# Performance work log

Measured on AMD Instinct MI355X. Metric: run time of the kernel, lower is better.

The kernel has to match this reference:

```python
import jax, jax.numpy as jnp
import numpy as np

C = 343.0      # speed of sound (init kwarg c)
F = 16         # number of frequency channels (len(omega))
H = 128        # MLP hidden width
N = 131072     # collocation points


def _mlp(coords, W1, b1, W2, b2, W3, b3):
    # coords: [..., 3] -> [..., 2F] (first F = real part, last F = imag part)
    h = jnp.tanh(coords @ W1 + b1)
    h = jnp.tanh(h @ W2 + b2)
    return h @ W3 + b3


def setup_inputs() -> dict:
    key = jax.random.key(0)
    ks = jax.random.split(key, 4)
    inputs = jax.random.normal(ks[0], (N, 3), dtype=jnp.float32)
    # omega = 2*pi*f for f = 100..1600 Hz (matches init kwarg list)
    omega = 2.0 * jnp.pi * 100.0 * jnp.arange(1, F + 1, dtype=jnp.float32)
    s_in = 1.0 / np.sqrt(3.0)
    s_h = 1.0 / np.sqrt(float(H))
    W1 = jax.random.normal(ks[1], (3, H), dtype=jnp.float32) * s_in
    b1 = jnp.zeros((H,), dtype=jnp.float32)
    W2 = jax.random.normal(ks[2], (H, H), dtype=jnp.float32) * s_h
    b2 = jnp.zeros((H,), dtype=jnp.float32)
    W3 = jax.random.normal(ks[3], (H, 2 * F), dtype=jnp.float32) * s_h
    b3 = jnp.zeros((2 * F,), dtype=jnp.float32)
    return {"inputs": inputs, "omega": omega, "W1": W1, "b1": b1,
            "W2": W2, "b2": b2, "W3": W3, "b3": b3}


def reference(inputs, omega, W1, b1, W2, b2, W3, b3):
    # Pointwise network R^3 -> R^{2F} (real/imag stacked).
    f = lambda c3: _mlp(c3, W1, b1, W2, b2, W3, b3)

    # u: complex pressure per point per frequency, [N, F]
    out = _mlp(inputs, W1, b1, W2, b2, W3, b3)           # [N, 2F]
    u = out[:, :F] + 1j * out[:, F:]

    # Full spatial Hessian per point via forward-over-reverse AD (fused
    # replacement for the torch per-channel autograd.grad loop).
    hess = jax.vmap(jax.jacfwd(jax.jacrev(f)))(inputs)   # [N, 2F, 3, 3]
    lap_ri = jnp.einsum('nfii->nf', hess)                # diagonal trace = Laplacian
    lap = lap_ri[:, :F] + 1j * lap_ri[:, F:]             # [N, F] complex

    # PDE residual skips channel 0, exactly as the torch loop (i+1 indexing).
    k2 = (omega[1:] / C) ** 2                            # [F-1]
    residual = lap[:, 1:] + k2 * u[:, 1:]                # [N, F-1]

    # mean over channels then over batch == global mean of |residual|^2
    return jnp.mean(jnp.abs(residual) ** 2)
```

## Files before the change

### kernel.cpp

```cpp
#include <hip/hip_runtime.h>
#include <math.h>

#ifndef __has_builtin
#define __has_builtin(x) 0
#endif

#define NPTS   131072
#define FCH    16
#define CSND   343.0f
#define PB     16
#define BLOCK  256
#define GRID   512
#define NBLK   (NPTS / PB)

typedef _Float16 half8 __attribute__((ext_vector_type(8)));
typedef _Float16 half2v __attribute__((ext_vector_type(2)));
typedef float    f32x4 __attribute__((ext_vector_type(4)));

static __device__ __forceinline__ unsigned pack2(float a, float b) {
#if __has_builtin(__builtin_amdgcn_cvt_pkrtz)
  return __builtin_bit_cast(unsigned, __builtin_amdgcn_cvt_pkrtz(a, b));
#else
  half2v v; v[0] = (_Float16)a; v[1] = (_Float16)b;
  return __builtin_bit_cast(unsigned, v);
#endif
}

static __device__ __forceinline__ float mytanh(float x) {
  float ax = fabsf(x);
  float e  = __expf(-2.0f * ax);
  float r  = (1.0f - e) * __builtin_amdgcn_rcpf(1.0f + e);
  return copysignf(r, x);
}


__global__ __launch_bounds__(BLOCK, 2) void helmholtz_kernel(
    const float* __restrict__ x,
    const float* __restrict__ omega,
    const float* __restrict__ W1,
    const float* __restrict__ b1,
    const float* __restrict__ W2,
    const float* __restrict__ b2,
    const float* __restrict__ W3,
    const float* __restrict__ b3,
    float* __restrict__ out)
{
  __shared__ unsigned s_w2t[128 * 64];
  __shared__ unsigned s_w3t[32 * 64];
  __shared__ unsigned s_A[80 * 64];

  const int tid  = threadIdx.x;
  const int w    = tid >> 6;
  const int l    = tid & 63;
  const int col  = l & 15;
  const int quad = l >> 4;

  for (int task = tid; task < 2048; task += BLOCK) {
    int n = task & 127, c = task >> 7;
    unsigned pk[4];
#pragma unroll
    for (int d = 0; d < 4; d++)
      pk[d] = pack2(W2[(8 * c + 2 * d) * 128 + n], W2[(8 * c + 2 * d + 1) * 128 + n]);
    uint4 q = make_uint4(pk[0], pk[1], pk[2], pk[3]);
    *(uint4*)&s_w2t[n * 64 + ((c ^ (n & 15)) << 2)] = q;
  }
  for (int task = tid; task < 512; task += BLOCK) {
    int n = task & 31, c = task >> 5;
    unsigned pk[4];
#pragma unroll
    for (int d = 0; d < 4; d++)
      pk[d] = pack2(W3[(8 * c + 2 * d) * 32 + n], W3[(8 * c + 2 * d + 1) * 32 + n]);
    uint4 q = make_uint4(pk[0], pk[1], pk[2], pk[3]);
    *(uint4*)&s_w3t[n * 64 + ((c ^ (n & 15)) << 2)] = q;
  }

  const int i2 = tid & 63;
  const float a0x = W1[2 * i2],       a0y = W1[128 + 2 * i2],  a0z = W1[256 + 2 * i2];
  const float a1x = W1[2 * i2 + 1],   a1y = W1[129 + 2 * i2],  a1z = W1[257 + 2 * i2];
  const float bb0 = b1[2 * i2],       bb1 = b1[2 * i2 + 1];
  const float wsq0 = a0x * a0x + a0y * a0y + a0z * a0z;
  const float wsq1 = a1x * a1x + a1y * a1y + a1z * a1z;
  const float b2r0 = b2[w * 32 + col];
  const float b2r1 = b2[w * 32 + 16 + col];
  const bool  activeE = (tid & 15) < 15;
  const int   cE = (tid & 15) + 1;
  float k2E = 0.0f, b3a = 0.0f, b3b = 0.0f;
  if (activeE) {
    float om = omega[cE] * (1.0f / CSND);
    k2E = om * om;
    b3a = b3[cE];
    b3b = b3[cE + 16];
  }

  float wsum = 0.0f;

  for (int blk = blockIdx.x; blk < NBLK; blk += gridDim.x) {
    const int pbase = blk * PB;
    __syncthreads();

#pragma unroll
    for (int it = 0; it < 4; it++) {
      int p = (tid >> 6) * 4 + it;
      const float* xp = x + (size_t)(pbase + p) * 3;
      float x0 = xp[0], x1 = xp[1], x2 = xp[2];
      float z0 = fmaf(x0, a0x, fmaf(x1, a0y, fmaf(x2, a0z, bb0)));
      float z1 = fmaf(x0, a1x, fmaf(x1, a1y, fmaf(x2, a1z, bb1)));
      float t0 = mytanh(z0), t1 = mytanh(z1);
      float s0 = 1.0f - t0 * t0, s1 = 1.0f - t1 * t1;
      unsigned u_h  = pack2(t0, t1);
      unsigned u_d0 = pack2(s0 * a0x, s1 * a1x);
      unsigned u_d1 = pack2(s0 * a0y, s1 * a1y);
      unsigned u_d2 = pack2(s0 * a0z, s1 * a1z);
      unsigned u_c  = pack2(-2.0f * t0 * s0 * wsq0, -2.0f * t1 * s1 * wsq1);
      int dcol = (((i2 >> 2) ^ p) << 2) + (i2 & 3);
      s_A[(p)      * 64 + dcol] = u_h;
      s_A[(16 + p) * 64 + dcol] = u_d0;
      s_A[(32 + p) * 64 + dcol] = u_d1;
      s_A[(48 + p) * 64 + dcol] = u_d2;
      s_A[(64 + p) * 64 + dcol] = u_c;
    }
    __syncthreads();

    f32x4 acc[5][2];
#pragma unroll
    for (int mt = 0; mt < 5; mt++)
#pragma unroll
      for (int ntl = 0; ntl < 2; ntl++)
        acc[mt][ntl] = (f32x4){0.0f, 0.0f, 0.0f, 0.0f};

    half8 bfrag[2][4];
#pragma unroll
    for (int ntl = 0; ntl < 2; ntl++) {
      int n = (2 * w + ntl) * 16 + col;
#pragma unroll
      for (int ks = 0; ks < 4; ks++) {
        int c = (ks * 4 + quad) ^ (n & 15);
        bfrag[ntl][ks] = *(const half8*)&s_w2t[n * 64 + (c << 2)];
      }
    }
#pragma unroll
    for (int mt = 0; mt < 5; mt++) {
      int m = mt * 16 + col;
#pragma unroll
      for (int ks = 0; ks < 4; ks++) {
        int c = (ks * 4 + quad) ^ (m & 15);
        half8 af = *(const half8*)&s_A[m * 64 + (c << 2)];
        acc[mt][0] = __builtin_amdgcn_mfma_f32_16x16x32_f16(af, bfrag[0][ks], acc[mt][0], 0, 0, 0);
        acc[mt][1] = __builtin_amdgcn_mfma_f32_16x16x32_f16(af, bfrag[1][ks], acc[mt][1], 0, 0, 0);
      }
    }
    __syncthreads();

    {
      _Float16* hg = (_Float16*)s_A;
#pragma unroll
      for (int ntl = 0; ntl < 2; ntl++) {
        int j = (2 * w + ntl) * 16 + col;
        int chunkj = j >> 3;
        float b2v = ntl ? b2r1 : b2r0;
#pragma unroll
        for (int r = 0; r < 4; r++) {
          int p = quad * 4 + r;
          float z2 = acc[0][ntl][r] + b2v;
          float d0 = acc[1][ntl][r], d1 = acc[2][ntl][r], d2 = acc[3][ntl][r];
          float Av = acc[4][ntl][r];
          float t2 = mytanh(z2);
          float s2 = 1.0f - t2 * t2;
          float g  = s2 * (Av - 2.0f * t2 * (d0 * d0 + d1 * d1 + d2 * d2));
          int base = ((chunkj ^ p) << 3) + (j & 7);
          hg[p * 128 + base]        = (_Float16)t2;
          hg[(16 + p) * 128 + base] = (_Float16)g;
        }
      }
    }
    __syncthreads();

    {
      int mtp = w >> 1, ntp = w & 1;
      int mrow = mtp * 16 + col;
      int n    = ntp * 16 + col;
      f32x4 dacc = (f32x4){0.0f, 0.0f, 0.0f, 0.0f};
#pragma unroll
      for (int ks = 0; ks < 4; ks++) {
        int ca = (ks * 4 + quad) ^ (mrow & 15);
        half8 af = *(const half8*)&s_A[mrow * 64 + (ca << 2)];
        int cb = (ks * 4 + quad) ^ (n & 15);
        half8 bf = *(const half8*)&s_w3t[n * 64 + (cb << 2)];
        dacc = __builtin_amdgcn_mfma_f32_16x16x32_f16(af, bf, dacc, 0, 0, 0);
      }
      float* ylds = (float*)&s_A[2048];
      int base = mtp ? 528 : 0;
#pragma unroll
      for (int r = 0; r < 4; r++) {
        int p = quad * 4 + r;
        ylds[base + p * 33 + ntp * 16 + col] = dacc[r];
      }
    }
    __syncthreads();

    if (activeE) {
      const float* ylds = (const float*)&s_A[2048];
      int p = tid >> 4;
      float yre = ylds[p * 33 + cE] + b3a;
      float yim = ylds[p * 33 + cE + 16] + b3b;
      float lre = ylds[528 + p * 33 + cE];
      float lim = ylds[528 + p * 33 + cE + 16];
      float re = fmaf(k2E, yre, lre);
      float im = fmaf(k2E, yim, lim);
      wsum += re * re + im * im;
    }
  }

#pragma unroll
  for (int off = 32; off > 0; off >>= 1)
    wsum += __shfl_down(wsum, off, 64);
  if (l == 0)
    atomicAdd(out, wsum * (1.0f / ((float)NPTS * (float)(FCH - 1))));
}

extern "C" void kernel_launch(void* const* d_in, const int* in_sizes, int n_in,
                              void* d_out, int out_size, void* d_ws, size_t ws_size,
                              hipStream_t stream) {
  const float* x     = (const float*)d_in[0];
  const float* omega = (const float*)d_in[1];
  const float* W1    = (const float*)d_in[2];
  const float* b1    = (const float*)d_in[3];
  const float* W2    = (const float*)d_in[4];
  const float* b2    = (const float*)d_in[5];
  const float* W3    = (const float*)d_in[6];
  const float* b3    = (const float*)d_in[7];
  float* out = (float*)d_out;

  (void)hipMemsetAsync(out, 0, sizeof(float), stream);
  helmholtz_kernel<<<GRID, BLOCK, 0, stream>>>(x, omega, W1, b1, W2, b2, W3, b3, out);
}
```

Before: 130.6 us.

## Keep W2/W3 MFMA fragments in registers and split LDS buffers for occupancy

Loads the W2 and W3 weight fragments straight from global memory into per-thread fp16 registers, so they are no longer staged through shared memory. This removes the LDS weight tables and their per-iteration fragment reads. Separate buffers for the hidden/gradient tile and the output tile replace the reuse of s_A, which lets two __syncthreads per iteration be dropped. Launch bounds move to 4 blocks per CU and the grid doubles, trading higher register pressure for occupancy.

```diff
diff --git a/kernel.cpp b/kernel.cpp
--- a/kernel.cpp
+++ b/kernel.cpp
@@ -10,7 +10,7 @@
 #define CSND   343.0f
 #define PB     16
 #define BLOCK  256
-#define GRID   512
+#define GRID   1024
 #define NBLK   (NPTS / PB)
 
 typedef _Float16 half8 __attribute__((ext_vector_type(8)));
@@ -34,7 +34,7 @@
 }
 
 
-__global__ __launch_bounds__(BLOCK, 2) void helmholtz_kernel(
+__global__ __launch_bounds__(BLOCK, 4) void helmholtz_kernel(
     const float* __restrict__ x,
     const float* __restrict__ omega,
     const float* __restrict__ W1,
@@ -45,34 +45,15 @@
     const float* __restrict__ b3,
     float* __restrict__ out)
 {
-  __shared__ unsigned s_w2t[128 * 64];
-  __shared__ unsigned s_w3t[32 * 64];
   __shared__ unsigned s_A[80 * 64];
+  __shared__ unsigned s_HG[32 * 64];
+  __shared__ float    s_Y[2 * 16 * 33];
 
   const int tid  = threadIdx.x;
   const int w    = tid >> 6;
   const int l    = tid & 63;
   const int col  = l & 15;
   const int quad = l >> 4;
-
-  for (int task = tid; task < 2048; task += BLOCK) {
-    int n = task & 127, c = task >> 7;
-    unsigned pk[4];
-#pragma unroll
-    for (int d = 0; d < 4; d++)
-      pk[d] = pack2(W2[(8 * c + 2 * d) * 128 + n], W2[(8 * c + 2 * d + 1) * 128 + n]);
-    uint4 q = make_uint4(pk[0], pk[1], pk[2], pk[3]);
-    *(uint4*)&s_w2t[n * 64 + ((c ^ (n & 15)) << 2)] = q;
-  }
-  for (int task = tid; task < 512; task += BLOCK) {
-    int n = task & 31, c = task >> 5;
-    unsigned pk[4];
-#pragma unroll
-    for (int d = 0; d < 4; d++)
-      pk[d] = pack2(W3[(8 * c + 2 * d) * 32 + n], W3[(8 * c + 2 * d + 1) * 32 + n]);
-    uint4 q = make_uint4(pk[0], pk[1], pk[2], pk[3]);
-    *(uint4*)&s_w3t[n * 64 + ((c ^ (n & 15)) << 2)] = q;
-  }
 
   const int i2 = tid & 63;
   const float a0x = W1[2 * i2],       a0y = W1[128 + 2 * i2],  a0z = W1[256 + 2 * i2];
@@ -80,6 +61,33 @@
   const float bb0 = b1[2 * i2],       bb1 = b1[2 * i2 + 1];
   const float wsq0 = a0x * a0x + a0y * a0y + a0z * a0z;
   const float wsq1 = a1x * a1x + a1y * a1y + a1z * a1z;
+
+  half8 w2f[2][4];
+#pragma unroll
+  for (int ntl = 0; ntl < 2; ntl++) {
+    const int n = (2 * w + ntl) * 16 + col;
+#pragma unroll
+    for (int ks = 0; ks < 4; ks++) {
+      half8 f;
+#pragma unroll
+      for (int j = 0; j < 8; j++)
+        f[j] = (_Float16)W2[(ks * 32 + (quad << 3) + j) * 128 + n];
+      w2f[ntl][ks] = f;
+    }
+  }
+  half8 w3f[4];
+  {
+    const int n = (w & 1) * 16 + col;
+#pragma unroll
+    for (int ks = 0; ks < 4; ks++) {
+      half8 f;
+#pragma unroll
+      for (int j = 0; j < 8; j++)
+        f[j] = (_Float16)W3[(ks * 32 + (quad << 3) + j) * 32 + n];
+      w3f[ks] = f;
+    }
+  }
+
   const float b2r0 = b2[w * 32 + col];
   const float b2r1 = b2[w * 32 + 16 + col];
   const bool  activeE = (tid & 15) < 15;
@@ -96,11 +104,10 @@
 
   for (int blk = blockIdx.x; blk < NBLK; blk += gridDim.x) {
     const int pbase = blk * PB;
-    __syncthreads();
 
 #pragma unroll
     for (int it = 0; it < 4; it++) {
-      int p = (tid >> 6) * 4 + it;
+      int p = w * 4 + it;
       const float* xp = x + (size_t)(pbase + p) * 3;
       float x0 = xp[0], x1 = xp[1], x2 = xp[2];
       float z0 = fmaf(x0, a0x, fmaf(x1, a0y, fmaf(x2, a0z, bb0)));
@@ -128,31 +135,20 @@
       for (int ntl = 0; ntl < 2; ntl++)
         acc[mt][ntl] = (f32x4){0.0f, 0.0f, 0.0f, 0.0f};
 
-    half8 bfrag[2][4];
-#pragma unroll
-    for (int ntl = 0; ntl < 2; ntl++) {
-      int n = (2 * w + ntl) * 16 + col;
-#pragma unroll
-      for (int ks = 0; ks < 4; ks++) {
-        int c = (ks * 4 + quad) ^ (n & 15);
-        bfrag[ntl][ks] = *(const half8*)&s_w2t[n * 64 + (c << 2)];
-      }
-    }
 #pragma unroll
     for (int mt = 0; mt < 5; mt++) {
       int m = mt * 16 + col;
 #pragma unroll
       for (int ks = 0; ks < 4; ks++) {
-        int c = (ks * 4 + quad) ^ (m & 15);
+        int c = (ks * 4 + quad) ^ col;
         half8 af = *(const half8*)&s_A[m * 64 + (c << 2)];
-        acc[mt][0] = __builtin_amdgcn_mfma_f32_16x16x32_f16(af, bfrag[0][ks], acc[mt][0], 0, 0, 0);
-        acc[mt][1] = __builtin_amdgcn_mfma_f32_16x16x32_f16(af, bfrag[1][ks], acc[mt][1], 0, 0, 0);
-      }
-    }
-    __syncthreads();
+        acc[mt][0] = __builtin_amdgcn_mfma_f32_16x16x32_f16(af, w2f[0][ks], acc[mt][0], 0, 0, 0);
+        acc[mt][1] = __builtin_amdgcn_mfma_f32_16x16x32_f16(af, w2f[1][ks], acc[mt][1], 0, 0, 0);
+      }
+    }
 
     {
-      _Float16* hg = (_Float16*)s_A;
+      _Float16* hg = (_Float16*)s_HG;
 #pragma unroll
       for (int ntl = 0; ntl < 2; ntl++) {
         int j = (2 * w + ntl) * 16 + col;
@@ -178,33 +174,28 @@
     {
       int mtp = w >> 1, ntp = w & 1;
       int mrow = mtp * 16 + col;
-      int n    = ntp * 16 + col;
       f32x4 dacc = (f32x4){0.0f, 0.0f, 0.0f, 0.0f};
 #pragma unroll
       for (int ks = 0; ks < 4; ks++) {
-        int ca = (ks * 4 + quad) ^ (mrow & 15);
-        half8 af = *(const half8*)&s_A[mrow * 64 + (ca << 2)];
-        int cb = (ks * 4 + quad) ^ (n & 15);
-        half8 bf = *(const half8*)&s_w3t[n * 64 + (cb << 2)];
-        dacc = __builtin_amdgcn_mfma_f32_16x16x32_f16(af, bf, dacc, 0, 0, 0);
-      }
-      float* ylds = (float*)&s_A[2048];
+        int ca = (ks * 4 + quad) ^ col;
+        half8 af = *(const half8*)&s_HG[mrow * 64 + (ca << 2)];
+        dacc = __builtin_amdgcn_mfma_f32_16x16x32_f16(af, w3f[ks], dacc, 0, 0, 0);
+      }
       int base = mtp ? 528 : 0;
 #pragma unroll
       for (int r = 0; r < 4; r++) {
         int p = quad * 4 + r;
-        ylds[base + p * 33 + ntp * 16 + col] = dacc[r];
+        s_Y[base + p * 33 + ntp * 16 + col] = dacc[r];
       }
     }
     __syncthreads();
 
     if (activeE) {
-      const float* ylds = (const float*)&s_A[2048];
       int p = tid >> 4;
-      float yre = ylds[p * 33 + cE] + b3a;
-      float yim = ylds[p * 33 + cE + 16] + b3b;
-      float lre = ylds[528 + p * 33 + cE];
-      float lim = ylds[528 + p * 33 + cE + 16];
+      float yre = s_Y[p * 33 + cE] + b3a;
+      float yim = s_Y[p * 33 + cE + 16] + b3b;
+      float lre = s_Y[528 + p * 33 + cE];
+      float lim = s_Y[528 + p * 33 + cE + 16];
       float re = fmaf(k2E, yre, lre);
       float im = fmaf(k2E, yim, lim);
       wsum += re * re + im * im;
```

Measured after the change: 152.6 us. +16.8%, slower.
